# Optimization experiments

Hardware: AMD Instinct MI355X
Metric: run time of the kernel (lower is better)

The kernel has to match this reference:

```python
import jax, jax.numpy as jnp
import numpy as np

N = 50000      # nodes
E = 800000     # edges
T = 3          # npass
ED = 64        # embedding_dim
NS = 23        # nshifts (arange(0.8, 3.0+1e-5, 0.1))
MD = NS + ED   # message_dim = 87
H = 200        # hidden width (hardcoded in module)
NMOL = 2048    # number of molecules (segments for final scatter)
RD = ED * (T + 1)  # readout input dim = 256
EPS = 1e-5

SHIFTS = jnp.asarray(np.arange(0.8, 3.0 + 1e-5, 0.1, dtype=np.float32))  # [23]


def setup_inputs() -> dict:
    key = jax.random.key(0)
    ks = jax.random.split(key, 32)
    inp = {
        'z_i': jax.random.randint(ks[0], (N,), 0, 10),
        'edge_index': jax.random.randint(ks[1], (2, E), 0, N),
        'dist_ij': jax.random.uniform(ks[2], (E, 1), dtype=jnp.float32) * 2.2 + 0.8,
        'mol_ind': jnp.sort(jax.random.randint(ks[3], (N,), 0, NMOL)),
        'emb': jax.random.normal(ks[4], (10, ED), dtype=jnp.float32),
        # per-pass update MLP params, stacked over T
        'up_bn_g': jnp.ones((T, MD), jnp.float32),
        'up_bn_b': jnp.zeros((T, MD), jnp.float32),
        'up_w1': jax.random.normal(ks[5], (T, MD, H), jnp.float32) * 0.05,
        'up_b1': jnp.zeros((T, H), jnp.float32),
        'up_w2': jax.random.normal(ks[6], (T, H, H), jnp.float32) * 0.05,
        'up_b2': jnp.zeros((T, H), jnp.float32),
        'up_w3': jax.random.normal(ks[7], (T, H, H), jnp.float32) * 0.05,
        'up_b3': jnp.zeros((T, H), jnp.float32),
        'up_w4': jax.random.normal(ks[8], (T, H, ED), jnp.float32) * 0.05,
        'up_b4': jnp.zeros((T, ED), jnp.float32),
        # readout MLP params
        'ro_bn_g': jnp.ones((RD,), jnp.float32),
        'ro_bn_b': jnp.zeros((RD,), jnp.float32),
        'ro_w1': jax.random.normal(ks[9], (RD, H), jnp.float32) * 0.05,
        'ro_b1': jnp.zeros((H,), jnp.float32),
        'ro_w2': jax.random.normal(ks[10], (H, H), jnp.float32) * 0.05,
        'ro_b2': jnp.zeros((H,), jnp.float32),
        'ro_w3': jax.random.normal(ks[11], (H, H), jnp.float32) * 0.05,
        'ro_b3': jnp.zeros((H,), jnp.float32),
        'ro_w4': jax.random.normal(ks[12], (H, 1), jnp.float32) * 0.05,
        'ro_b4': jnp.zeros((1,), jnp.float32),  # bias filled to 0 in __init__
    }
    return inp


def batchnorm(x, g, b):
    # BatchNorm1d in training mode: batch statistics, biased variance
    mu = jnp.mean(x, axis=0)
    var = jnp.mean(jnp.square(x - mu), axis=0)
    return (x - mu) * jax.lax.rsqrt(var + EPS) * g + b


def mlp(x, g, b, w1, b1, w2, b2, w3, b3, w4, b4):
    x = batchnorm(x, g, b)
    x = jax.nn.relu(x @ w1 + b1)
    x = jax.nn.relu(x @ w2 + b2)
    x = jax.nn.relu(x @ w3 + b3)
    return x @ w4 + b4


def reference(z_i, edge_index, dist_ij, mol_ind, emb,
              up_bn_g, up_bn_b, up_w1, up_b1, up_w2, up_b2, up_w3, up_b3, up_w4, up_b4,
              ro_bn_g, ro_bn_b, ro_w1, ro_b1, ro_w2, ro_b2, ro_w3, ro_b3, ro_w4, ro_b4):
    e_source, e_sink = edge_index[0], edge_index[1]
    rbf_ij = jnp.exp(-jnp.square(dist_ij - SHIFTS[None, :]))  # [E, NS]
    x_i = emb[z_i]                                            # [N, ED]
    x_list = [x_i]
    for t in range(T):
        m_ij = jnp.concatenate([rbf_ij, x_i[e_sink]], axis=1)  # [E, MD] gather
        m_i = jax.ops.segment_sum(m_ij, e_source, num_segments=N)  # scatter-sum
        x_i = x_i + 0.1 * mlp(m_i, up_bn_g[t], up_bn_b[t],
                              up_w1[t], up_b1[t], up_w2[t], up_b2[t],
                              up_w3[t], up_b3[t], up_w4[t], up_b4[t])
        x_list.append(x_i)
    x_all = jnp.concatenate(x_list, axis=1)  # [N, RD]
    y_i = mlp(x_all, ro_bn_g, ro_bn_b, ro_w1, ro_b1, ro_w2, ro_b2, ro_w3, ro_b3, ro_w4, ro_b4)
    y = jax.ops.segment_sum(y_i, mol_ind, num_segments=NMOL)  # [NMOL, 1]
    return y
```

## Files before the change

kernel.cpp:

```cpp
#include <hip/hip_runtime.h>
#include <hip/hip_bf16.h>
#include <type_traits>

#define NN 50000
#define NP 50048
#define EE 800000
#define TT 3
#define ED 64
#define NS 23
#define MD 87
#define HH 200
#define NMOL 2048
#define RD 256

#define SP 216
#define NPB2 512
#define SNB ((NN + 255) / 256)

typedef __attribute__((ext_vector_type(8))) short short8b;
typedef __attribute__((ext_vector_type(4))) short short4b;
typedef __attribute__((ext_vector_type(4))) float f32x4;

__device__ __forceinline__ unsigned short f2bf(float f) {
  unsigned u = __float_as_uint(f);
  return (unsigned short)((u + 0x7fffu + ((u >> 16) & 1u)) >> 16);
}
__device__ __forceinline__ float ubf2f(unsigned short h) {
  return __uint_as_float(((unsigned)h) << 16);
}
__device__ __forceinline__ float bfp2f(unsigned p) {
  return __uint_as_float(p << 16) + __uint_as_float(p & 0xffff0000u);
}
__device__ __forceinline__ unsigned packsplit(float v) {
  unsigned short h = f2bf(v);
  unsigned short l = f2bf(v - ubf2f(h));
  return (unsigned)h | ((unsigned)l << 16);
}

struct WD { const float* src; short* dh; short* dl; int K, N, Kpad, Npad, T; };
struct WDs { WD d[5]; };

__global__ __launch_bounds__(256) void wprep_kernel(WDs W) {
  WD w = W.d[blockIdx.y];
  int per = w.Npad * w.Kpad;
  int total = w.T * per;
  for (int idx = blockIdx.x * 256 + threadIdx.x; idx < total; idx += gridDim.x * 256) {
    int t = idx / per;
    int r = idx - t * per;
    int n = r / w.Kpad;
    int k = r - n * w.Kpad;
    float v = 0.f;
    if (k < w.K && n < w.N) v = w.src[((size_t)t * w.K + k) * w.N + n];
    unsigned short h = f2bf(v);
    unsigned short l = f2bf(v - ubf2f(h));
    w.dh[idx] = (short)h;
    w.dl[idx] = (short)l;
  }
}

__global__ __launch_bounds__(256) void wscale_kernel(const float* __restrict__ wsrc,
                                                     const float* __restrict__ na,
                                                     const float* __restrict__ nb,
                                                     const float* __restrict__ bsrc,
                                                     int K, int Kpad,
                                                     short* __restrict__ wsh,
                                                     short* __restrict__ wsl,
                                                     float* __restrict__ bc) {
  int n = blockIdx.x;
  int k = threadIdx.x;
  float contrib = 0.f;
  if (n < HH && k < K) {
    float w = wsrc[(size_t)k * HH + n];
    float v = na[k] * w;
    unsigned short h = f2bf(v);
    wsh[(size_t)n * Kpad + k] = (short)h;
    wsl[(size_t)n * Kpad + k] = (short)f2bf(v - ubf2f(h));
    contrib = nb[k] * w;
  } else if (k < Kpad) {
    wsh[(size_t)n * Kpad + k] = 0;
    wsl[(size_t)n * Kpad + k] = 0;
  }
  __shared__ float sh[256];
  sh[k] = contrib;
  __syncthreads();
  for (int off = 128; off > 0; off >>= 1) {
    if (k < off) sh[k] += sh[k + off];
    __syncthreads();
  }
  if (k == 0) bc[n] = (n < HH ? bsrc[n] : 0.f) + sh[0];
}

__global__ __launch_bounds__(256) void emb_kernel(const int* __restrict__ z,
                                                  const float* __restrict__ emb,
                                                  unsigned* __restrict__ xp,
                                                  short* __restrict__ xq) {
  int idx = blockIdx.x * 256 + threadIdx.x;
  if (idx >= NN * ED) return;
  int i = idx >> 6, d = idx & 63;
  unsigned pk = packsplit(emb[z[i] * ED + d]);
  xp[(size_t)i * RD + d] = pk;
  xq[(size_t)i * RD + d] = (short)(pk & 0xffffu);
}

__global__ __launch_bounds__(256) void hist_kernel(const int* __restrict__ src,
                                                   int* __restrict__ deg) {
  int e = blockIdx.x * 256 + threadIdx.x;
  if (e < EE) atomicAdd(&deg[src[e]], 1);
}

__global__ __launch_bounds__(256) void scanA_kernel(const int* __restrict__ deg,
                                                    int* __restrict__ Psum) {
  int i = blockIdx.x * 256 + threadIdx.x;
  int v = (i < NN) ? deg[i] : 0;
#pragma unroll
  for (int off = 32; off > 0; off >>= 1) v += __shfl_down(v, off, 64);
  __shared__ int ws[4];
  if ((threadIdx.x & 63) == 0) ws[threadIdx.x >> 6] = v;
  __syncthreads();
  if (threadIdx.x == 0) Psum[blockIdx.x] = ws[0] + ws[1] + ws[2] + ws[3];
}

__global__ __launch_bounds__(256) void scanB_kernel(const int* __restrict__ Psum,
                                                    int* __restrict__ Poff) {
  __shared__ int sh[256];
  int t = threadIdx.x;
  int v = (t < SNB) ? Psum[t] : 0;
  sh[t] = v;
  __syncthreads();
  for (int off = 1; off < 256; off <<= 1) {
    int u = (t >= off) ? sh[t - off] : 0;
    __syncthreads();
    sh[t] += u;
    __syncthreads();
  }
  if (t < SNB) Poff[t] = sh[t] - v;
}

__global__ __launch_bounds__(256) void scanC_kernel(const int* __restrict__ deg,
                                                    const int* __restrict__ Poff,
                                                    int* __restrict__ offs,
                                                    int* __restrict__ cursor) {
  __shared__ int sh[256];
  int t = threadIdx.x;
  int i = blockIdx.x * 256 + t;
  int v = (i < NN) ? deg[i] : 0;
  sh[t] = v;
  __syncthreads();
  for (int off = 1; off < 256; off <<= 1) {
    int u = (t >= off) ? sh[t - off] : 0;
    __syncthreads();
    sh[t] += u;
    __syncthreads();
  }
  int excl = Poff[blockIdx.x] + sh[t] - v;
  if (i < NN) {
    offs[i] = excl;
    cursor[i] = excl;
    if (i == NN - 1) offs[NN] = excl + v;
  }
}

__global__ __launch_bounds__(256) void scatter_kernel(const int* __restrict__ src,
                                                      const int* __restrict__ snk,
                                                      const float* __restrict__ dist,
                                                      int* __restrict__ cursor,
                                                      int* __restrict__ ssink,
                                                      float* __restrict__ sdist) {
  int e = blockIdx.x * 256 + threadIdx.x;
  if (e >= EE) return;
  int p = atomicAdd(&cursor[src[e]], 1);
  ssink[p] = snk[e];
  sdist[p] = dist[e];
}

__global__ __launch_bounds__(256) void gather_kernel(const int* __restrict__ offs,
                                                     const int* __restrict__ ssink,
                                                     const float* __restrict__ sdist,
                                                     const short* __restrict__ xq,
                                                     int toff, short* __restrict__ mh) {
  int node = blockIdx.x * 4 + (threadIdx.x >> 6);
  int lane = threadIdx.x & 63;
  if (node >= NN) return;
  float shift = (float)(0.8 + 0.1 * (double)lane);
  int e0 = offs[node], e1 = offs[node + 1];
  float ax0 = 0.f, ax1 = 0.f, ar0 = 0.f, ar1 = 0.f;
  int j = e0;
  for (; j + 4 <= e1; j += 4) {
    int s0 = ssink[j], s1 = ssink[j + 1], s2 = ssink[j + 2], s3 = ssink[j + 3];
    float d0 = sdist[j], d1 = sdist[j + 1], d2 = sdist[j + 2], d3 = sdist[j + 3];
    float x0 = ubf2f((unsigned short)xq[(size_t)s0 * RD + toff + lane]);
    float x1 = ubf2f((unsigned short)xq[(size_t)s1 * RD + toff + lane]);
    float x2 = ubf2f((unsigned short)xq[(size_t)s2 * RD + toff + lane]);
    float x3 = ubf2f((unsigned short)xq[(size_t)s3 * RD + toff + lane]);
    ax0 += x0 + x2;
    ax1 += x1 + x3;
    if (lane < NS) {
      float u0 = d0 - shift, u1 = d1 - shift, u2 = d2 - shift, u3 = d3 - shift;
      ar0 += __expf(-u0 * u0) + __expf(-u2 * u2);
      ar1 += __expf(-u1 * u1) + __expf(-u3 * u3);
    }
  }
  for (; j < e1; j++) {
    int s = ssink[j];
    float d = sdist[j];
    ax0 += ubf2f((unsigned short)xq[(size_t)s * RD + toff + lane]);
    if (lane < NS) {
      float u = d - shift;
      ar0 += __expf(-u * u);
    }
  }
  float accx = ax0 + ax1, accr = ar0 + ar1;
  if (lane < NS) mh[(size_t)node * 96 + lane] = (short)f2bf(accr);
  mh[(size_t)node * 96 + NS + lane] = (short)f2bf(accx);
}

template <int LD>
__global__ __launch_bounds__(256) void colstats_s16_kernel(const short* __restrict__ X,
                                                           float* __restrict__ P) {
  constexpr int CG = LD / 8;
  constexpr int RPB = 256 / CG;
  const int t = threadIdx.x;
  const int cg = t % CG, rin = t / CG;
  float s[8] = {0, 0, 0, 0, 0, 0, 0, 0}, q[8] = {0, 0, 0, 0, 0, 0, 0, 0};
  if (rin < RPB) {
    for (int r = blockIdx.x * RPB + rin; r < NN; r += gridDim.x * RPB) {
      union { uint4 v; short e[8]; } u;
      u.v = *(const uint4*)(X + (size_t)r * LD + cg * 8);
#pragma unroll
      for (int e = 0; e < 8; e++) {
        float f = ubf2f((unsigned short)u.e[e]);
        s[e] += f;
        q[e] += f * f;
      }
    }
  }
  __shared__ float sh[256][16];
#pragma unroll
  for (int e = 0; e < 8; e++) { sh[t][e] = s[e]; sh[t][8 + e] = q[e]; }
  __syncthreads();
  if (rin == 0) {
    for (int rr = 1; rr < RPB; rr++) {
      const float* o = sh[rr * CG + cg];
#pragma unroll
      for (int e = 0; e < 8; e++) { s[e] += o[e]; q[e] += o[8 + e]; }
    }
    float* Pb = P + blockIdx.x * 512;
#pragma unroll
    for (int e = 0; e < 8; e++) {
      Pb[cg * 8 + e] = s[e];
      Pb[256 + cg * 8 + e] = q[e];
    }
  }
}

__global__ __launch_bounds__(256) void bnfinal2_kernel(const float* __restrict__ P, int nblk,
                                                       const float* __restrict__ g,
                                                       const float* __restrict__ b, int ncols,
                                                       float* __restrict__ na,
                                                       float* __restrict__ nb) {
  int c = blockIdx.x;
  int t = threadIdx.x;
  float s = 0.f, q = 0.f;
  for (int i = t; i < nblk; i += 256) {
    s += P[i * 512 + c];
    q += P[i * 512 + 256 + c];
  }
#pragma unroll
  for (int off = 32; off > 0; off >>= 1) {
    s += __shfl_down(s, off, 64);
    q += __shfl_down(q, off, 64);
  }
  __shared__ float ws[4], wq[4];
  if ((t & 63) == 0) { ws[t >> 6] = s; wq[t >> 6] = q; }
  __syncthreads();
  if (t == 0) {
    s = ws[0] + ws[1] + ws[2] + ws[3];
    q = wq[0] + wq[1] + wq[2] + wq[3];
    if (c < ncols) {
      float mean = s / (float)NN;
      float var = q / (float)NN - mean * mean;
      float a = g[c] * rsqrtf(var + 1e-5f);
      na[c] = a;
      nb[c] = b[c] - mean * a;
    } else {
      na[c] = 0.f;
      nb[c] = 0.f;
    }
  }
}

template <bool READOUT>
__global__ __launch_bounds__(512, 4) void fused_kernel(
    const short* __restrict__ Agh, int glda,
    const short* __restrict__ W1h, const short* __restrict__ W1l,
    const short* __restrict__ W2h, const short* __restrict__ W2l,
    const short* __restrict__ W3h, const short* __restrict__ W3l,
    const short* __restrict__ W4h, const short* __restrict__ W4l,
    const float* __restrict__ b1, const float* __restrict__ b2,
    const float* __restrict__ b3, const float* __restrict__ b4,
    unsigned* __restrict__ xp, short* __restrict__ xq, int t,
    const float* __restrict__ w4ro, const int* __restrict__ mol,
    float* __restrict__ out) {
  __shared__ short ldsH[64 * SP + 16];
  const int tid = threadIdx.x;
  const int wave = tid >> 6, lane = tid & 63, ln = lane & 15, quad = lane >> 4;
  const int bm = blockIdx.x * 64;
  const int ntile = (wave < 5) ? 2 : 1;
  const int n0col = ((wave < 5) ? 2 * wave : wave + 5) * 16;

  if (tid < 16) ldsH[64 * SP + tid] = 0;

  f32x4 acc[4][2];

  auto layer = [&](auto ga_tag, const short* __restrict__ Wh,
                   const short* __restrict__ Wl, int Kpad, int KP) {
    constexpr bool GA = decltype(ga_tag)::value;
#pragma unroll
    for (int i = 0; i < 4; i++)
#pragma unroll
      for (int j = 0; j < 2; j++) acc[i][j] = (f32x4){0.f, 0.f, 0.f, 0.f};
    for (int k0 = 0; k0 < KP; k0 += 32) {
      short8b ah[4], bh[2], bl[2];
#pragma unroll
      for (int i = 0; i < 4; i++) {
        int r = i * 16 + ln;
        if constexpr (GA)
          ah[i] = *(const short8b*)(Agh + (size_t)(bm + r) * glda + k0 + quad * 8);
        else
          ah[i] = *(const short8b*)(ldsH + r * SP + k0 + quad * 8);
      }
#pragma unroll
      for (int j = 0; j < 2; j++)
        if (j < ntile) {
          const size_t o = (size_t)(n0col + j * 16 + ln) * Kpad + k0 + quad * 8;
          bh[j] = *(const short8b*)(Wh + o);
          bl[j] = *(const short8b*)(Wl + o);
        }
#pragma unroll
      for (int j = 0; j < 2; j++)
        if (j < ntile)
#pragma unroll
          for (int i = 0; i < 4; i++) {
            acc[i][j] = __builtin_amdgcn_mfma_f32_16x16x32_bf16(ah[i], bh[j], acc[i][j], 0, 0, 0);
            acc[i][j] = __builtin_amdgcn_mfma_f32_16x16x32_bf16(ah[i], bl[j], acc[i][j], 0, 0, 0);
          }
    }
  };

  auto epi = [&](const float* __restrict__ bias) {
    __syncthreads();
#pragma unroll
    for (int i = 0; i < 4; i++)
#pragma unroll
      for (int j = 0; j < 2; j++)
        if (j < ntile)
#pragma unroll
          for (int r = 0; r < 4; r++) {
            int row = i * 16 + quad * 4 + r;
            int col = n0col + j * 16 + ln;
            float v = acc[i][j][r] + (col < HH ? bias[col] : 0.f);
            v = fmaxf(v, 0.f);
            ldsH[row * SP + col] = (short)f2bf(v);
          }
    ldsH[(tid >> 3) * SP + 208 + (tid & 7)] = 0;
    __syncthreads();
  };

  if (!READOUT) {
    layer(std::true_type{}, W1h, W1l, 96, 96);
    epi(b1);
    layer(std::false_type{}, W2h, W2l, 224, 224);
    epi(b2);
    layer(std::false_type{}, W3h, W3l, 224, 224);
    epi(b3);
    const int wm4 = wave & 1, wn4 = wave >> 1;
    f32x4 a4[2];
#pragma unroll
    for (int i = 0; i < 2; i++) a4[i] = (f32x4){0.f, 0.f, 0.f, 0.f};
    for (int k0 = 0; k0 < 224; k0 += 32) {
      short8b ah[2], bh, bl;
#pragma unroll
      for (int i = 0; i < 2; i++) {
        int r = wm4 * 32 + i * 16 + ln;
        ah[i] = *(const short8b*)(ldsH + r * SP + k0 + quad * 8);
      }
      const size_t o = (size_t)(wn4 * 16 + ln) * 224 + k0 + quad * 8;
      bh = *(const short8b*)(W4h + o);
      bl = *(const short8b*)(W4l + o);
#pragma unroll
      for (int i = 0; i < 2; i++) {
        a4[i] = __builtin_amdgcn_mfma_f32_16x16x32_bf16(ah[i], bh, a4[i], 0, 0, 0);
        a4[i] = __builtin_amdgcn_mfma_f32_16x16x32_bf16(ah[i], bl, a4[i], 0, 0, 0);
      }
    }
#pragma unroll
    for (int i = 0; i < 2; i++)
#pragma unroll
      for (int r = 0; r < 4; r++) {
        int grow = bm + wm4 * 32 + i * 16 + quad * 4 + r;
        int col = wn4 * 16 + ln;
        if (grow < NN) {
          float v = a4[i][r] + b4[col];
          size_t base = (size_t)grow * RD;
          float old = bfp2f(xp[base + (size_t)t * ED + col]);
          unsigned pk = packsplit(old + 0.1f * v);
          xp[base + (size_t)(t + 1) * ED + col] = pk;
          xq[base + (size_t)(t + 1) * ED + col] = (short)(pk & 0xffffu);
        }
      }
  } else {
    layer(std::true_type{}, W1h, W1l, 256, 256);
    epi(b1);
    layer(std::false_type{}, W2h, W2l, 224, 224);
    epi(b2);
    layer(std::false_type{}, W3h, W3l, 224, 224);
    epi(b3);
    int row = tid >> 3;
    int grow = bm + row;
    float s = 0.f;
    for (int c = (tid & 7); c < HH; c += 8)
      s += ubf2f((unsigned short)ldsH[row * SP + c]) * w4ro[c];
    s += __shfl_xor(s, 1, 64);
    s += __shfl_xor(s, 2, 64);
    s += __shfl_xor(s, 4, 64);
    if ((tid & 7) == 0 && grow < NN) atomicAdd(&out[mol[grow]], s + b4[0]);
  }
}

extern "C" void kernel_launch(void* const* d_in, const int* in_sizes, int n_in,
                              void* d_out, int out_size, void* d_ws, size_t ws_size,
                              hipStream_t stream) {
  const int* z_i = (const int*)d_in[0];
  const int* e_src = (const int*)d_in[1];
  const int* e_snk = ((const int*)d_in[1]) + EE;
  const float* dist = (const float*)d_in[2];
  const int* mol = (const int*)d_in[3];
  const float* emb = (const float*)d_in[4];
  const float* up_bn_g = (const float*)d_in[5];
  const float* up_bn_b = (const float*)d_in[6];
  const float* up_w1 = (const float*)d_in[7];
  const float* up_b1 = (const float*)d_in[8];
  const float* up_w2 = (const float*)d_in[9];
  const float* up_b2 = (const float*)d_in[10];
  const float* up_w3 = (const float*)d_in[11];
  const float* up_b3 = (const float*)d_in[12];
  const float* up_w4 = (const float*)d_in[13];
  const float* up_b4 = (const float*)d_in[14];
  const float* ro_bn_g = (const float*)d_in[15];
  const float* ro_bn_b = (const float*)d_in[16];
  const float* ro_w1 = (const float*)d_in[17];
  const float* ro_b1 = (const float*)d_in[18];
  const float* ro_w2 = (const float*)d_in[19];
  const float* ro_b2 = (const float*)d_in[20];
  const float* ro_w3 = (const float*)d_in[21];
  const float* ro_b3 = (const float*)d_in[22];
  const float* ro_w4 = (const float*)d_in[23];
  const float* ro_b4 = (const float*)d_in[24];
  float* out = (float*)d_out;

  char* p = (char*)d_ws;
  auto alloc = [&](size_t bytes) {
    void* r = (void*)p;
    p += (bytes + 255) & ~(size_t)255;
    return r;
  };
  unsigned* x_p = (unsigned*)alloc((size_t)NN * RD * 4);
  short* x_q = (short*)alloc((size_t)NP * RD * 2);
  short* mh = (short*)alloc((size_t)NP * 96 * 2);
  int* ssink = (int*)alloc((size_t)EE * 4);
  float* sdist = (float*)alloc((size_t)EE * 4);
  int* offs = (int*)alloc((size_t)(NN + 1) * 4);
  int* deg = (int*)alloc((size_t)NN * 4);
  int* cursor = (int*)alloc((size_t)NN * 4);
  int* Psum = (int*)alloc((size_t)SNB * 4);
  int* Poff = (int*)alloc((size_t)SNB * 4);
  float* P = (float*)alloc((size_t)NPB2 * 512 * 4);
  float* na = (float*)alloc(256 * 4);
  float* nb = (float*)alloc(256 * 4);
  float* b1c = (float*)alloc(208 * 4);
  short* w1sh = (short*)alloc((size_t)208 * 96 * 2);
  short* w1sl = (short*)alloc((size_t)208 * 96 * 2);
  short* r1sh = (short*)alloc((size_t)208 * 256 * 2);
  short* r1sl = (short*)alloc((size_t)208 * 256 * 2);
  short* w2h = (short*)alloc((size_t)TT * 208 * 224 * 2);
  short* w2l = (short*)alloc((size_t)TT * 208 * 224 * 2);
  short* w3h = (short*)alloc((size_t)TT * 208 * 224 * 2);
  short* w3l = (short*)alloc((size_t)TT * 208 * 224 * 2);
  short* w4h = (short*)alloc((size_t)TT * 64 * 224 * 2);
  short* w4l = (short*)alloc((size_t)TT * 64 * 224 * 2);
  short* r2h = (short*)alloc((size_t)208 * 224 * 2);
  short* r2l = (short*)alloc((size_t)208 * 224 * 2);
  short* r3h = (short*)alloc((size_t)208 * 224 * 2);
  short* r3l = (short*)alloc((size_t)208 * 224 * 2);

  hipMemsetAsync(deg, 0, (size_t)NN * 4, stream);
  hipMemsetAsync(out, 0, (size_t)NMOL * 4, stream);

  WDs descs;
  descs.d[0] = {up_w2, w2h, w2l, HH, HH, 224, 208, TT};
  descs.d[1] = {up_w3, w3h, w3l, HH, HH, 224, 208, TT};
  descs.d[2] = {up_w4, w4h, w4l, HH, ED, 224, 64, TT};
  descs.d[3] = {ro_w2, r2h, r2l, HH, HH, 224, 208, 1};
  descs.d[4] = {ro_w3, r3h, r3l, HH, HH, 224, 208, 1};
  wprep_kernel<<<dim3(546, 5), 256, 0, stream>>>(descs);

  emb_kernel<<<(NN * ED + 255) / 256, 256, 0, stream>>>(z_i, emb, x_p, x_q);
  hist_kernel<<<(EE + 255) / 256, 256, 0, stream>>>(e_src, deg);
  scanA_kernel<<<SNB, 256, 0, stream>>>(deg, Psum);
  scanB_kernel<<<1, 256, 0, stream>>>(Psum, Poff);
  scanC_kernel<<<SNB, 256, 0, stream>>>(deg, Poff, offs, cursor);
  scatter_kernel<<<(EE + 255) / 256, 256, 0, stream>>>(e_src, e_snk, dist, cursor, ssink, sdist);

  const int gM = NP / 64;

  for (int t = 0; t < TT; t++) {
    gather_kernel<<<(NN + 3) / 4, 256, 0, stream>>>(offs, ssink, sdist, x_q, t * ED, mh);
    colstats_s16_kernel<96><<<NPB2, 256, 0, stream>>>(mh, P);
    bnfinal2_kernel<<<256, 256, 0, stream>>>(P, NPB2, up_bn_g + t * MD, up_bn_b + t * MD, MD,
                                             na, nb);
    wscale_kernel<<<208, 256, 0, stream>>>(up_w1 + (size_t)t * MD * HH, na, nb,
                                           up_b1 + t * HH, MD, 96, w1sh, w1sl, b1c);
    fused_kernel<false><<<gM, 512, 0, stream>>>(
        mh, 96, w1sh, w1sl,
        w2h + (size_t)t * 208 * 224, w2l + (size_t)t * 208 * 224,
        w3h + (size_t)t * 208 * 224, w3l + (size_t)t * 208 * 224,
        w4h + (size_t)t * 64 * 224, w4l + (size_t)t * 64 * 224,
        b1c, up_b2 + t * HH, up_b3 + t * HH, up_b4 + t * ED,
        x_p, x_q, t, nullptr, nullptr, nullptr);
  }

  colstats_s16_kernel<256><<<NPB2, 256, 0, stream>>>(x_q, P);
  bnfinal2_kernel<<<256, 256, 0, stream>>>(P, NPB2, ro_bn_g, ro_bn_b, RD, na, nb);
  wscale_kernel<<<208, 256, 0, stream>>>(ro_w1, na, nb, ro_b1, RD, 256, r1sh, r1sl, b1c);
  fused_kernel<true><<<gM, 512, 0, stream>>>(
      x_q, 256, r1sh, r1sl,
      r2h, r2l, r3h, r3l, nullptr, nullptr,
      b1c, ro_b2, ro_b3, ro_b4,
      nullptr, nullptr, 0, ro_w4, mol, out);

  (void)in_sizes; (void)n_in; (void)out_size; (void)ws_size;
}
```

Baseline: 685.0 us.

## Pack weights in MFMA fragment order and drop low-bf16 term for hidden layers

```diff
diff --git a/kernel.cpp b/kernel.cpp
--- a/kernel.cpp
+++ b/kernel.cpp
@@ -37,24 +37,29 @@
   return (unsigned)h | ((unsigned)l << 16);
 }
 
-struct WD { const float* src; short* dh; short* dl; int K, N, Kpad, Npad, T; };
+struct WD { const float* src; short* dst; int K, N, Kpad, Npad, T; };
 struct WDs { WD d[5]; };
 
 __global__ __launch_bounds__(256) void wprep_kernel(WDs W) {
   WD w = W.d[blockIdx.y];
+  int KB = w.Kpad >> 5, NT = w.Npad >> 4;
   int per = w.Npad * w.Kpad;
   int total = w.T * per;
   for (int idx = blockIdx.x * 256 + threadIdx.x; idx < total; idx += gridDim.x * 256) {
     int t = idx / per;
     int r = idx - t * per;
-    int n = r / w.Kpad;
-    int k = r - n * w.Kpad;
+    int e = r & 7, lane = (r >> 3) & 63;
+    int blk = r >> 9;
+    int kb = blk % KB, tile = blk / KB;
+    int ln = lane & 15, quad = lane >> 4;
+    int n = tile * 16 + ln, k = kb * 32 + quad * 8 + e;
     float v = 0.f;
     if (k < w.K && n < w.N) v = w.src[((size_t)t * w.K + k) * w.N + n];
     unsigned short h = f2bf(v);
     unsigned short l = f2bf(v - ubf2f(h));
-    w.dh[idx] = (short)h;
-    w.dl[idx] = (short)l;
+    size_t base = ((size_t)(t * NT + tile) * KB + kb) * 1024;
+    w.dst[base + lane * 8 + e] = (short)h;
+    w.dst[base + 512 + lane * 8 + e] = (short)l;
   }
 }
 
@@ -63,22 +68,27 @@
                                                      const float* __restrict__ nb,
                                                      const float* __restrict__ bsrc,
                                                      int K, int Kpad,
-                                                     short* __restrict__ wsh,
-                                                     short* __restrict__ wsl,
+                                                     short* __restrict__ wsp,
                                                      float* __restrict__ bc) {
   int n = blockIdx.x;
   int k = threadIdx.x;
+  int KB = Kpad >> 5;
+  int tile = n >> 4, ln = n & 15;
   float contrib = 0.f;
-  if (n < HH && k < K) {
-    float w = wsrc[(size_t)k * HH + n];
-    float v = na[k] * w;
+  if (k < Kpad) {
+    float v = 0.f;
+    if (n < HH && k < K) {
+      float w = wsrc[(size_t)k * HH + n];
+      v = na[k] * w;
+      contrib = nb[k] * w;
+    }
     unsigned short h = f2bf(v);
-    wsh[(size_t)n * Kpad + k] = (short)h;
-    wsl[(size_t)n * Kpad + k] = (short)f2bf(v - ubf2f(h));
-    contrib = nb[k] * w;
-  } else if (k < Kpad) {
-    wsh[(size_t)n * Kpad + k] = 0;
-    wsl[(size_t)n * Kpad + k] = 0;
+    unsigned short l = f2bf(v - ubf2f(h));
+    int kb = k >> 5, quad = (k & 31) >> 3, e = k & 7;
+    int lane = quad * 16 + ln;
+    size_t base = ((size_t)tile * KB + kb) * 1024;
+    wsp[base + lane * 8 + e] = (short)h;
+    wsp[base + 512 + lane * 8 + e] = (short)l;
   }
   __shared__ float sh[256];
   sh[k] = contrib;
@@ -292,10 +302,9 @@
 template <bool READOUT>
 __global__ __launch_bounds__(512, 4) void fused_kernel(
     const short* __restrict__ Agh, int glda,
-    const short* __restrict__ W1h, const short* __restrict__ W1l,
-    const short* __restrict__ W2h, const short* __restrict__ W2l,
-    const short* __restrict__ W3h, const short* __restrict__ W3l,
-    const short* __restrict__ W4h, const short* __restrict__ W4l,
+    const short* __restrict__ W1p, int KB1,
+    const short* __restrict__ W2p, const short* __restrict__ W3p,
+    const short* __restrict__ W4p,
     const float* __restrict__ b1, const float* __restrict__ b2,
     const float* __restrict__ b3, const float* __restrict__ b4,
     unsigned* __restrict__ xp, short* __restrict__ xq, int t,
@@ -306,20 +315,23 @@
   const int wave = tid >> 6, lane = tid & 63, ln = lane & 15, quad = lane >> 4;
   const int bm = blockIdx.x * 64;
   const int ntile = (wave < 5) ? 2 : 1;
-  const int n0col = ((wave < 5) ? 2 * wave : wave + 5) * 16;
+  const int tile0 = (wave < 5) ? 2 * wave : wave + 5;
+  const int n0col = tile0 * 16;
 
   if (tid < 16) ldsH[64 * SP + tid] = 0;
 
   f32x4 acc[4][2];
 
-  auto layer = [&](auto ga_tag, const short* __restrict__ Wh,
-                   const short* __restrict__ Wl, int Kpad, int KP) {
+  auto layer = [&](auto ga_tag, auto terms_tag, const short* __restrict__ Wp,
+                   int KB, int KP) {
     constexpr bool GA = decltype(ga_tag)::value;
+    constexpr int TERMS = decltype(terms_tag)::value;
 #pragma unroll
     for (int i = 0; i < 4; i++)
 #pragma unroll
       for (int j = 0; j < 2; j++) acc[i][j] = (f32x4){0.f, 0.f, 0.f, 0.f};
     for (int k0 = 0; k0 < KP; k0 += 32) {
+      const int kb = k0 >> 5;
       short8b ah[4], bh[2], bl[2];
 #pragma unroll
       for (int i = 0; i < 4; i++) {
@@ -332,9 +344,9 @@
 #pragma unroll
       for (int j = 0; j < 2; j++)
         if (j < ntile) {
-          const size_t o = (size_t)(n0col + j * 16 + ln) * Kpad + k0 + quad * 8;
-          bh[j] = *(const short8b*)(Wh + o);
-          bl[j] = *(const short8b*)(Wl + o);
+          const short* bp = Wp + ((size_t)((tile0 + j) * KB + kb)) * 1024 + lane * 8;
+          bh[j] = *(const short8b*)bp;
+          if constexpr (TERMS == 2) bl[j] = *(const short8b*)(bp + 512);
         }
 #pragma unroll
       for (int j = 0; j < 2; j++)
@@ -342,7 +354,9 @@
 #pragma unroll
           for (int i = 0; i < 4; i++) {
             acc[i][j] = __builtin_amdgcn_mfma_f32_16x16x32_bf16(ah[i], bh[j], acc[i][j], 0, 0, 0);
-            acc[i][j] = __builtin_amdgcn_mfma_f32_16x16x32_bf16(ah[i], bl[j], acc[i][j], 0, 0, 0);
+            if constexpr (TERMS == 2)
+              acc[i][j] =
+                  __builtin_amdgcn_mfma_f32_16x16x32_bf16(ah[i], bl[j], acc[i][j], 0, 0, 0);
           }
     }
   };
@@ -366,27 +380,31 @@
     __syncthreads();
   };
 
+  using one_t = std::integral_constant<int, 1>;
+  using two_t = std::integral_constant<int, 2>;
+
   if (!READOUT) {
-    layer(std::true_type{}, W1h, W1l, 96, 96);
+    layer(std::true_type{}, two_t{}, W1p, KB1, 96);
     epi(b1);
-    layer(std::false_type{}, W2h, W2l, 224, 224);
+    layer(std::false_type{}, one_t{}, W2p, 7, 224);
     epi(b2);
-    layer(std::false_type{}, W3h, W3l, 224, 224);
+    layer(std::false_type{}, one_t{}, W3p, 7, 224);
     epi(b3);
     const int wm4 = wave & 1, wn4 = wave >> 1;
     f32x4 a4[2];
 #pragma unroll
     for (int i = 0; i < 2; i++) a4[i] = (f32x4){0.f, 0.f, 0.f, 0.f};
     for (int k0 = 0; k0 < 224; k0 += 32) {
+      const int kb = k0 >> 5;
       short8b ah[2], bh, bl;
 #pragma unroll
       for (int i = 0; i < 2; i++) {
         int r = wm4 * 32 + i * 16 + ln;
         ah[i] = *(const short8b*)(ldsH + r * SP + k0 + quad * 8);
       }
-      const size_t o = (size_t)(wn4 * 16 + ln) * 224 + k0 + quad * 8;
-      bh = *(const short8b*)(W4h + o);
-      bl = *(const short8b*)(W4l + o);
+      const short* bp = W4p + ((size_t)(wn4 * 7 + kb)) * 1024 + lane * 8;
+      bh = *(const short8b*)bp;
+      bl = *(const short8b*)(bp + 512);
 #pragma unroll
       for (int i = 0; i < 2; i++) {
         a4[i] = __builtin_amdgcn_mfma_f32_16x16x32_bf16(ah[i], bh, a4[i], 0, 0, 0);
@@ -409,11 +427,11 @@
         }
       }
   } else {
-    layer(std::true_type{}, W1h, W1l, 256, 256);
+    layer(std::true_type{}, two_t{}, W1p, KB1, 256);
     epi(b1);
-    layer(std::false_type{}, W2h, W2l, 224, 224);
+    layer(std::false_type{}, one_t{}, W2p, 7, 224);
     epi(b2);
-    layer(std::false_type{}, W3h, W3l, 224, 224);
+    layer(std::false_type{}, one_t{}, W3p, 7, 224);
     epi(b3);
     int row = tid >> 3;
     int grow = bm + row;
@@ -478,30 +496,23 @@
   float* na = (float*)alloc(256 * 4);
   float* nb = (float*)alloc(256 * 4);
   float* b1c = (float*)alloc(208 * 4);
-  short* w1sh = (short*)alloc((size_t)208 * 96 * 2);
-  short* w1sl = (short*)alloc((size_t)208 * 96 * 2);
-  short* r1sh = (short*)alloc((size_t)208 * 256 * 2);
-  short* r1sl = (short*)alloc((size_t)208 * 256 * 2);
-  short* w2h = (short*)alloc((size_t)TT * 208 * 224 * 2);
-  short* w2l = (short*)alloc((size_t)TT * 208 * 224 * 2);
-  short* w3h = (short*)alloc((size_t)TT * 208 * 224 * 2);
-  short* w3l = (short*)alloc((size_t)TT * 208 * 224 * 2);
-  short* w4h = (short*)alloc((size_t)TT * 64 * 224 * 2);
-  short* w4l = (short*)alloc((size_t)TT * 64 * 224 * 2);
-  short* r2h = (short*)alloc((size_t)208 * 224 * 2);
-  short* r2l = (short*)alloc((size_t)208 * 224 * 2);
-  short* r3h = (short*)alloc((size_t)208 * 224 * 2);
-  short* r3l = (short*)alloc((size_t)208 * 224 * 2);
+  short* w1sp = (short*)alloc((size_t)13 * 3 * 1024 * 2);
+  short* r1sp = (short*)alloc((size_t)13 * 8 * 1024 * 2);
+  short* w2p = (short*)alloc((size_t)TT * 13 * 7 * 1024 * 2);
+  short* w3p = (short*)alloc((size_t)TT * 13 * 7 * 1024 * 2);
+  short* w4p = (short*)alloc((size_t)TT * 4 * 7 * 1024 * 2);
+  short* r2p = (short*)alloc((size_t)13 * 7 * 1024 * 2);
+  short* r3p = (short*)alloc((size_t)13 * 7 * 1024 * 2);
 
   hipMemsetAsync(deg, 0, (size_t)NN * 4, stream);
   hipMemsetAsync(out, 0, (size_t)NMOL * 4, stream);
 
   WDs descs;
-  descs.d[0] = {up_w2, w2h, w2l, HH, HH, 224, 208, TT};
-  descs.d[1] = {up_w3, w3h, w3l, HH, HH, 224, 208, TT};
-  descs.d[2] = {up_w4, w4h, w4l, HH, ED, 224, 64, TT};
-  descs.d[3] = {ro_w2, r2h, r2l, HH, HH, 224, 208, 1};
-  descs.d[4] = {ro_w3, r3h, r3l, HH, HH, 224, 208, 1};
+  descs.d[0] = {up_w2, w2p, HH, HH, 224, 208, TT};
+  descs.d[1] = {up_w3, w3p, HH, HH, 224, 208, TT};
+  descs.d[2] = {up_w4, w4p, HH, ED, 224, 64, TT};
+  descs.d[3] = {ro_w2, r2p, HH, HH, 224, 208, 1};
+  descs.d[4] = {ro_w3, r3p, HH, HH, 224, 208, 1};
   wprep_kernel<<<dim3(546, 5), 256, 0, stream>>>(descs);
 
   emb_kernel<<<(NN * ED + 255) / 256, 256, 0, stream>>>(z_i, emb, x_p, x_q);
@@ -519,22 +530,21 @@
     bnfinal2_kernel<<<256, 256, 0, stream>>>(P, NPB2, up_bn_g + t * MD, up_bn_b + t * MD, MD,
                                              na, nb);
     wscale_kernel<<<208, 256, 0, stream>>>(up_w1 + (size_t)t * MD * HH, na, nb,
-                                           up_b1 + t * HH, MD, 96, w1sh, w1sl, b1c);
+                                           up_b1 + t * HH, MD, 96, w1sp, b1c);
     fused_kernel<false><<<gM, 512, 0, stream>>>(
-        mh, 96, w1sh, w1sl,
-        w2h + (size_t)t * 208 * 224, w2l + (size_t)t * 208 * 224,
-        w3h + (size_t)t * 208 * 224, w3l + (size_t)t * 208 * 224,
-        w4h + (size_t)t * 64 * 224, w4l + (size_t)t * 64 * 224,
+        mh, 96, w1sp, 3,
+        w2p + (size_t)t * 13 * 7 * 1024, w3p + (size_t)t * 13 * 7 * 1024,
+        w4p + (size_t)t * 4 * 7 * 1024,
         b1c, up_b2 + t * HH, up_b3 + t * HH, up_b4 + t * ED,
         x_p, x_q, t, nullptr, nullptr, nullptr);
   }
 
   colstats_s16_kernel<256><<<NPB2, 256, 0, stream>>>(x_q, P);
   bnfinal2_kernel<<<256, 256, 0, stream>>>(P, NPB2, ro_bn_g, ro_bn_b, RD, na, nb);
-  wscale_kernel<<<208, 256, 0, stream>>>(ro_w1, na, nb, ro_b1, RD, 256, r1sh, r1sl, b1c);
+  wscale_kernel<<<208, 256, 0, stream>>>(ro_w1, na, nb, ro_b1, RD, 256, r1sp, b1c);
   fused_kernel<true><<<gM, 512, 0, stream>>>(
-      x_q, 256, r1sh, r1sl,
-      r2h, r2l, r3h, r3l, nullptr, nullptr,
+      x_q, 256, r1sp, 8,
+      r2p, r3p, nullptr,
       b1c, ro_b2, ro_b3, ro_b4,
       nullptr, nullptr, 0, ro_w4, mol, out);
 
```

New measurement: 613.2 us. 1.12x faster.
